# Kernel optimization log

Measured on AMD Instinct MI355X. Metric: run time of the kernel, lower is better.

## Reference

```python
import jax, jax.numpy as jnp
import numpy as np

M = 41
RHO = M / 2.0          # rho=-1 -> M/2
OVERLAPS = 40
STRIDES = 40
N_FFT = OVERLAPS + STRIDES   # 80
HOP = STRIDES                # 40

def _get_index():
    S = []
    for n1 in range(-(M // 2), M // 2):
        for n2 in range(-(M // 2), M // 2):
            if abs(n1 * n2) <= RHO * (M // 2):
                S.append((n1, n2))
    return np.asarray(S, dtype=np.int64)

IDX = _get_index()          # [K,2], K=1600
N1 = IDX[:, 0]
N2 = IDX[:, 1]
K = len(IDX)

def setup_inputs() -> dict:
    key = jax.random.key(0)
    ks = jax.random.split(key, 7)
    b, L, m = 2, 2080, 2
    return {
        "x_real": jax.random.normal(ks[0], (b, L, m), jnp.float32),
        "x_imag": jax.random.normal(ks[1], (b, L, m), jnp.float32),
        "task_info": jax.random.uniform(ks[2], (b, 4), jnp.float32),
        "w_real": jax.random.normal(ks[3], (K,), jnp.float32) * 0.02,
        "w_imag": jax.random.normal(ks[4], (K,), jnp.float32) * 0.02,
        "b_real": jax.random.normal(ks[5], (1,), jnp.float32) * 0.02,
        "b_imag": jax.random.normal(ks[6], (1,), jnp.float32) * 0.02,
    }

def _stft(x):
    # x: [b, L, m] complex -> [b, T, F, m]; rectangular window, center=False
    L = x.shape[1]
    T = (L - N_FFT) // HOP + 1
    idx = np.arange(T)[:, None] * HOP + np.arange(N_FFT)[None, :]
    frames = x[:, idx, :]                      # [b, T, F, m]
    return jnp.fft.fft(frames, axis=2)

def _istft(X, L):
    # X: [b, T, F, m] -> [b, L, m] via overlap-add, rect-window normalization
    frames = jnp.fft.ifft(X, axis=2)
    b, T, F, m = X.shape
    idx = (np.arange(T)[:, None] * HOP + np.arange(F)[None, :]).reshape(-1)
    y = jnp.zeros((b, L, m), X.dtype).at[:, idx, :].add(frames.reshape(b, -1, m))
    cov = np.zeros(L)
    np.add.at(cov, idx, 1.0)
    cov = jnp.asarray(np.where(cov > 0, cov, 1.0), jnp.float32)
    return y / cov[None, :, None]

def reference(x_real, x_imag, task_info, w_real, w_imag, b_real, b_imag):
    x = x_real + 1j * x_imag                   # [b, L, m] complex64
    b, L, m = x.shape
    # get_power: launch power (dBm in task_info[:,0]) -> mW per mode
    P = jnp.power(10.0, task_info[:, 0] / 10.0) / m   # [b]
    X = _stft(x)                               # [b, T, F, m]
    F = N_FFT
    f = np.arange(F)
    g1 = (f[None, :] - N1[:, None]) % F        # [K, F] : torch.roll(X, n1, dims=2)
    g12 = (f[None, :] - (N1 + N2)[:, None]) % F
    g2 = (f[None, :] - N2[:, None]) % F
    # A_k = roll(X,n1) * conj(roll(X,n1+n2))   -> [b, T, K, F, m]
    A = X[:, :, g1, :] * jnp.conj(X[:, :, g12, :])
    A = A + jnp.roll(A, 1, axis=1)             # + previous frame (circular)
    E = A * X[:, :, g2, :]                     # [b, T, K, F, m]
    w = (w_real + 1j * w_imag).astype(E.dtype)
    bias = (b_real[0] + 1j * b_imag[0]).astype(E.dtype)
    delta = jnp.einsum('btkfm,k->btfm', E, w) + bias   # ComplexLinear(K,1)
    d = _istft(delta, L)                       # [b, L, m]
    out = x + d * P[:, None, None].astype(d.dtype)
    return out[:, OVERLAPS // 2: L - OVERLAPS // 2, :]
```

## Files before the change

### kernel.cpp

```cpp
#include <hip/hip_runtime.h>
#include <math.h>

#define BATCH 2
#define LLEN  2080
#define MCH   2
#define TT    51
#define FF    80
#define HOP   40
#define KW    1600
#define OUTL  2040
#define NT    640
#define PI_F  3.14159265358979323846f

__global__ __launch_bounds__(NT) void fused_kernel(
    const float* __restrict__ xr, const float* __restrict__ xi,
    const float* __restrict__ wr, const float* __restrict__ wi,
    const float* __restrict__ br, const float* __restrict__ bi,
    float2* __restrict__ Fr)
{
    __shared__ float2 xs[2 * FF];
    __shared__ float2 tw[FF];
    __shared__ float2 Yt2[2 * FF];
    __shared__ float2 Yp[FF];
    __shared__ float2 Wsh[KW];
    __shared__ float2 Zall[40][2 * FF];
    __shared__ float2 dvec[FF];

    float2* red  = &Zall[0][0];
    float2 (*redD)[FF] = (float2(*)[FF])&Zall[0][0];

    int tid = threadIdx.x;
    int bid = blockIdx.x;
    int b   = bid / (TT * MCH);
    int rem = bid % (TT * MCH);
    int t   = rem / MCH;
    int mi  = rem % MCH;
    int tp  = (t + TT - 1) % TT;

    if (tid < FF) {
        int g = (b * LLEN + t * HOP + tid) * MCH + mi;
        xs[tid] = make_float2(xr[g], xi[g]);
        float s, c;
        sincosf((2.0f * PI_F / FF) * (float)tid, &s, &c);
        tw[tid] = make_float2(c, s);
    } else if (tid < 2 * FF) {
        int j = tid - FF;
        int g = (b * LLEN + tp * HOP + j) * MCH + mi;
        xs[tid] = make_float2(xr[g], xi[g]);
    } else {
        for (int k = tid - 2 * FF; k < KW; k += NT - 2 * FF)
            Wsh[k] = make_float2(wr[k], wi[k]);
    }
    __syncthreads();

    {
        int o    = tid >> 2;
        int part = tid & 3;
        int ff   = o % FF;
        int frm  = o / FF;
        const float2* xb = &xs[frm * FF];
        float2 a = make_float2(0.f, 0.f);
        int j0 = part * 20;
        int r  = (ff * j0) % FF;
        for (int j = j0; j < j0 + 20; ++j) {
            float2 xv = xb[j];
            float2 tv = tw[r];
            a.x += xv.x * tv.x + xv.y * tv.y;
            a.y += xv.y * tv.x - xv.x * tv.y;
            r += ff; if (r >= FF) r -= FF;
        }
        red[part * 160 + o] = a;
    }
    __syncthreads();
    if (tid < 2 * FF) {
        float2 s = make_float2(0.f, 0.f);
        for (int p = 0; p < 4; ++p) {
            float2 v = red[p * 160 + tid];
            s.x += v.x; s.y += v.y;
        }
        if (tid < FF) {
            Yt2[tid + 20] = s;
            Yt2[(tid < 60) ? (tid + 100) : (tid - 60)] = s;
        } else {
            Yp[tid - FF] = s;
        }
    }
    __syncthreads();

    for (int i = 0; i < 5; ++i) {
        int zi = tid + i * NT;
        int jn = zi / FF;
        int g  = zi % FF;
        int n2 = jn - 20;
        int gm = g - n2; if (gm >= FF) gm -= FF; if (gm < 0) gm += FF;
        float2 a  = Yt2[g + 20], bm = Yt2[gm + 20];
        float2 cc = Yp[g],       dm = Yp[gm];
        float zre = a.x * bm.x + a.y * bm.y + cc.x * dm.x + cc.y * dm.y;
        float zim = a.y * bm.x - a.x * bm.y + cc.y * dm.x - cc.x * dm.y;
        float2 z = make_float2(zre, zim);
        Zall[jn][g + 20] = z;
        Zall[jn][(g < 60) ? (g + 100) : (g - 60)] = z;
    }
    __syncthreads();

    float2 o0, o1, o2, o3, o4;
    int jn, fb;
    {
        jn = tid >> 4;
        int fg = tid & 15;
        fb = fg * 5;
        const float2* zz = Zall[jn];

        float2 S0 = make_float2(0.f,0.f), S1 = S0, S2 = S0, S3 = S0, S4 = S0;
        float2 w0 = zz[fb + 40], w1 = zz[fb + 41], w2 = zz[fb + 42],
               w3 = zz[fb + 43], w4 = zz[fb + 44];
        #pragma unroll
        for (int jn1 = 0; jn1 < 40; ++jn1) {
            float2 wv = Wsh[jn1 * 40 + jn];
            S0.x += wv.x * w0.x - wv.y * w0.y;  S0.y += wv.x * w0.y + wv.y * w0.x;
            S1.x += wv.x * w1.x - wv.y * w1.y;  S1.y += wv.x * w1.y + wv.y * w1.x;
            S2.x += wv.x * w2.x - wv.y * w2.y;  S2.y += wv.x * w2.y + wv.y * w2.x;
            S3.x += wv.x * w3.x - wv.y * w3.y;  S3.y += wv.x * w3.y + wv.y * w3.x;
            S4.x += wv.x * w4.x - wv.y * w4.y;  S4.y += wv.x * w4.y + wv.y * w4.x;
            if (jn1 < 39) {
                float2 nv = zz[fb + 39 - jn1];
                w4 = w3; w3 = w2; w2 = w1; w1 = w0; w0 = nv;
            }
        }
        float2 y;
        y = Yt2[fb + 0 - jn + 40]; o0 = make_float2(y.x*S0.x - y.y*S0.y, y.x*S0.y + y.y*S0.x);
        y = Yt2[fb + 1 - jn + 40]; o1 = make_float2(y.x*S1.x - y.y*S1.y, y.x*S1.y + y.y*S1.x);
        y = Yt2[fb + 2 - jn + 40]; o2 = make_float2(y.x*S2.x - y.y*S2.y, y.x*S2.y + y.y*S2.x);
        y = Yt2[fb + 3 - jn + 40]; o3 = make_float2(y.x*S3.x - y.y*S3.y, y.x*S3.y + y.y*S3.x);
        y = Yt2[fb + 4 - jn + 40]; o4 = make_float2(y.x*S4.x - y.y*S4.y, y.x*S4.y + y.y*S4.x);
    }
    __syncthreads();
    redD[jn][fb + 0] = o0;
    redD[jn][fb + 1] = o1;
    redD[jn][fb + 2] = o2;
    redD[jn][fb + 3] = o3;
    redD[jn][fb + 4] = o4;
    __syncthreads();
    if (tid < FF) {
        float2 s = make_float2(br[0], bi[0]);
        for (int p = 0; p < 40; ++p) {
            float2 v = redD[p][tid];
            s.x += v.x; s.y += v.y;
        }
        dvec[tid] = s;
    }
    __syncthreads();

    {
        int j    = tid >> 3;
        int part = tid & 7;
        float2 a = make_float2(0.f, 0.f);
        int f0 = part * 10;
        int r  = (j * f0) % FF;
        for (int ff2 = f0; ff2 < f0 + 10; ++ff2) {
            float2 dv = dvec[ff2];
            float2 tv = tw[r];
            a.x += dv.x * tv.x - dv.y * tv.y;
            a.y += dv.x * tv.y + dv.y * tv.x;
            r += j; if (r >= FF) r -= FF;
        }
        red[part * FF + j] = a;
    }
    __syncthreads();
    if (tid < FF) {
        float2 s = make_float2(0.f, 0.f);
        for (int p = 0; p < 8; ++p) {
            float2 v = red[p * FF + tid];
            s.x += v.x; s.y += v.y;
        }
        s.x *= (1.0f / FF);
        s.y *= (1.0f / FF);
        Fr[((b * TT + t) * MCH + mi) * FF + tid] = s;
    }
}

__global__ void out_kernel(
    const float* __restrict__ xr, const float* __restrict__ xi,
    const float* __restrict__ ti, const float2* __restrict__ Fr,
    float* __restrict__ out, int out_size)
{
    int idx = blockIdx.x * blockDim.x + threadIdx.x;
    int tot = BATCH * OUTL * MCH;
    if (idx >= tot) return;
    int mi  = idx % MCH;
    int rem = idx / MCH;
    int lo  = rem % OUTL;
    int b   = rem / OUTL;
    int l   = lo + 20;

    float P = exp2f(ti[b * 4] * 0.33219280948873623f) * 0.5f;

    int t1 = l / HOP;
    int t0 = t1 - 1;
    float2 acc = make_float2(0.f, 0.f);
    float cov = 0.f;
    if (t1 <= TT - 1) {
        float2 v = Fr[((b * TT + t1) * MCH + mi) * FF + (l - HOP * t1)];
        acc.x += v.x; acc.y += v.y; cov += 1.f;
    }
    if (t0 >= 0) {
        float2 v = Fr[((b * TT + t0) * MCH + mi) * FF + (l - HOP * t0)];
        acc.x += v.x; acc.y += v.y; cov += 1.f;
    }
    float inv = 1.0f / cov;
    acc.x *= inv; acc.y *= inv;

    int gi = (b * LLEN + l) * MCH + mi;
    float outr = xr[gi] + acc.x * P;
    if (out_size == tot) {
        out[idx] = outr;
    } else {
        float outi = xi[gi] + acc.y * P;
        out[idx * 2]     = outr;
        out[idx * 2 + 1] = outi;
    }
}

extern "C" void kernel_launch(void* const* d_in, const int* in_sizes, int n_in,
                              void* d_out, int out_size, void* d_ws, size_t ws_size,
                              hipStream_t stream)
{
    const float* xr = (const float*)d_in[0];
    const float* xi = (const float*)d_in[1];
    const float* ti = (const float*)d_in[2];
    const float* wr = (const float*)d_in[3];
    const float* wi = (const float*)d_in[4];
    const float* br = (const float*)d_in[5];
    const float* bi = (const float*)d_in[6];

    float2* Fr = (float2*)d_ws;

    int nb = BATCH * TT * MCH;
    fused_kernel<<<nb, NT, 0, stream>>>(xr, xi, wr, wi, br, bi, Fr);

    int tot = BATCH * OUTL * MCH;
    out_kernel<<<(tot + 255) / 256, 256, 0, stream>>>(xr, xi, ti, Fr,
                                                      (float*)d_out, out_size);
}
```

Before: 16.96 us.

## Move inverse DFT into output kernel and use recurrence twiddles with shuffle reductions

The inverse DFT of each frame no longer runs in the fused kernel. The output kernel now computes it per output sample: two threads evaluate the two overlapping frames and combine their results with a lane shuffle. The forward DFT builds its twiddles by complex-rotation recurrence instead of reading a shared table, and reduces its partial sums with warp shuffles, which removes one barrier. The K reduction is split into two stages to shorten the serial loop. The aim is to cut barriers and serial work in the big kernel, at the cost of redundant 80-term sums in the second kernel and some recurrence rounding error.

```diff
diff --git a/kernel.cpp b/kernel.cpp
--- a/kernel.cpp
+++ b/kernel.cpp
@@ -10,24 +10,21 @@
 #define KW    1600
 #define OUTL  2040
 #define NT    640
+#define NB    (BATCH * TT * MCH)
 #define PI_F  3.14159265358979323846f
 
-__global__ __launch_bounds__(NT) void fused_kernel(
+__global__ __launch_bounds__(NT) void fused_k1(
     const float* __restrict__ xr, const float* __restrict__ xi,
     const float* __restrict__ wr, const float* __restrict__ wi,
     const float* __restrict__ br, const float* __restrict__ bi,
-    float2* __restrict__ Fr)
+    float2* __restrict__ dvec_g)
 {
     __shared__ float2 xs[2 * FF];
-    __shared__ float2 tw[FF];
     __shared__ float2 Yt2[2 * FF];
     __shared__ float2 Yp[FF];
     __shared__ float2 Wsh[KW];
     __shared__ float2 Zall[40][2 * FF];
-    __shared__ float2 dvec[FF];
-
-    float2* red  = &Zall[0][0];
-    float2 (*redD)[FF] = (float2(*)[FF])&Zall[0][0];
+    float2* flat = &Zall[0][0];
 
     int tid = threadIdx.x;
     int bid = blockIdx.x;
@@ -37,15 +34,10 @@
     int mi  = rem % MCH;
     int tp  = (t + TT - 1) % TT;
 
-    if (tid < FF) {
-        int g = (b * LLEN + t * HOP + tid) * MCH + mi;
-        xs[tid] = make_float2(xr[g], xi[g]);
-        float s, c;
-        sincosf((2.0f * PI_F / FF) * (float)tid, &s, &c);
-        tw[tid] = make_float2(c, s);
-    } else if (tid < 2 * FF) {
-        int j = tid - FF;
-        int g = (b * LLEN + tp * HOP + j) * MCH + mi;
+    if (tid < 2 * FF) {
+        int frm = tid / FF, j = tid % FF;
+        int tt  = frm == 0 ? t : tp;
+        int g = (b * LLEN + tt * HOP + j) * MCH + mi;
         xs[tid] = make_float2(xr[g], xi[g]);
     } else {
         for (int k = tid - 2 * FF; k < KW; k += NT - 2 * FF)
@@ -59,30 +51,36 @@
         int ff   = o % FF;
         int frm  = o / FF;
         const float2* xb = &xs[frm * FF];
+
+        int q = (ff * part) & 3;
+        float2 tv = (q == 0) ? make_float2(1.f, 0.f)
+                  : (q == 1) ? make_float2(0.f, -1.f)
+                  : (q == 2) ? make_float2(-1.f, 0.f)
+                  :            make_float2(0.f, 1.f);
+        float sp, cp;
+        sincosf(-(2.0f * PI_F / FF) * (float)ff, &sp, &cp);
+        float2 st = make_float2(cp, sp);
+
         float2 a = make_float2(0.f, 0.f);
-        int j0 = part * 20;
-        int r  = (ff * j0) % FF;
-        for (int j = j0; j < j0 + 20; ++j) {
+        int j = part * 20;
+        #pragma unroll 4
+        for (int i = 0; i < 20; ++i, ++j) {
             float2 xv = xb[j];
-            float2 tv = tw[r];
-            a.x += xv.x * tv.x + xv.y * tv.y;
-            a.y += xv.y * tv.x - xv.x * tv.y;
-            r += ff; if (r >= FF) r -= FF;
-        }
-        red[part * 160 + o] = a;
-    }
-    __syncthreads();
-    if (tid < 2 * FF) {
-        float2 s = make_float2(0.f, 0.f);
-        for (int p = 0; p < 4; ++p) {
-            float2 v = red[p * 160 + tid];
-            s.x += v.x; s.y += v.y;
-        }
-        if (tid < FF) {
-            Yt2[tid + 20] = s;
-            Yt2[(tid < 60) ? (tid + 100) : (tid - 60)] = s;
-        } else {
-            Yp[tid - FF] = s;
+            a.x += xv.x * tv.x - xv.y * tv.y;
+            a.y += xv.x * tv.y + xv.y * tv.x;
+            float nx = tv.x * st.x - tv.y * st.y;
+            tv.y = tv.x * st.y + tv.y * st.x;
+            tv.x = nx;
+        }
+        a.x += __shfl_xor(a.x, 1); a.y += __shfl_xor(a.y, 1);
+        a.x += __shfl_xor(a.x, 2); a.y += __shfl_xor(a.y, 2);
+        if (part == 0) {
+            if (o < FF) {
+                Yt2[o + 20] = a;
+                Yt2[(o < 60) ? (o + 100) : (o - 60)] = a;
+            } else {
+                Yp[o - FF] = a;
+            }
         }
     }
     __syncthreads();
@@ -135,89 +133,90 @@
         y = Yt2[fb + 4 - jn + 40]; o4 = make_float2(y.x*S4.x - y.y*S4.y, y.x*S4.y + y.y*S4.x);
     }
     __syncthreads();
-    redD[jn][fb + 0] = o0;
-    redD[jn][fb + 1] = o1;
-    redD[jn][fb + 2] = o2;
-    redD[jn][fb + 3] = o3;
-    redD[jn][fb + 4] = o4;
+    flat[jn * FF + fb + 0] = o0;
+    flat[jn * FF + fb + 1] = o1;
+    flat[jn * FF + fb + 2] = o2;
+    flat[jn * FF + fb + 3] = o3;
+    flat[jn * FF + fb + 4] = o4;
+    __syncthreads();
+
+    {
+        int f = tid % FF;
+        int p = tid / FF;
+        float2 s = make_float2(0.f, 0.f);
+        for (int q2 = 0; q2 < 5; ++q2) {
+            float2 v = flat[(p * 5 + q2) * FF + f];
+            s.x += v.x; s.y += v.y;
+        }
+        flat[3200 + p * FF + f] = s;
+    }
     __syncthreads();
     if (tid < FF) {
         float2 s = make_float2(br[0], bi[0]);
-        for (int p = 0; p < 40; ++p) {
-            float2 v = redD[p][tid];
+        for (int p = 0; p < 8; ++p) {
+            float2 v = flat[3200 + p * FF + tid];
             s.x += v.x; s.y += v.y;
         }
-        dvec[tid] = s;
-    }
-    __syncthreads();
-
-    {
-        int j    = tid >> 3;
-        int part = tid & 7;
-        float2 a = make_float2(0.f, 0.f);
-        int f0 = part * 10;
-        int r  = (j * f0) % FF;
-        for (int ff2 = f0; ff2 < f0 + 10; ++ff2) {
-            float2 dv = dvec[ff2];
-            float2 tv = tw[r];
-            a.x += dv.x * tv.x - dv.y * tv.y;
-            a.y += dv.x * tv.y + dv.y * tv.x;
-            r += j; if (r >= FF) r -= FF;
-        }
-        red[part * FF + j] = a;
-    }
-    __syncthreads();
-    if (tid < FF) {
-        float2 s = make_float2(0.f, 0.f);
-        for (int p = 0; p < 8; ++p) {
-            float2 v = red[p * FF + tid];
-            s.x += v.x; s.y += v.y;
-        }
-        s.x *= (1.0f / FF);
-        s.y *= (1.0f / FF);
-        Fr[((b * TT + t) * MCH + mi) * FF + tid] = s;
+        dvec_g[((b * TT + t) * MCH + mi) * FF + tid] = s;
     }
 }
 
-__global__ void out_kernel(
+__global__ void out_k2(
     const float* __restrict__ xr, const float* __restrict__ xi,
-    const float* __restrict__ ti, const float2* __restrict__ Fr,
+    const float* __restrict__ ti, const float2* __restrict__ dvec_g,
     float* __restrict__ out, int out_size)
 {
-    int idx = blockIdx.x * blockDim.x + threadIdx.x;
-    int tot = BATCH * OUTL * MCH;
-    if (idx >= tot) return;
-    int mi  = idx % MCH;
-    int rem = idx / MCH;
-    int lo  = rem % OUTL;
-    int b   = rem / OUTL;
-    int l   = lo + 20;
-
-    float P = exp2f(ti[b * 4] * 0.33219280948873623f) * 0.5f;
-
-    int t1 = l / HOP;
-    int t0 = t1 - 1;
-    float2 acc = make_float2(0.f, 0.f);
-    float cov = 0.f;
-    if (t1 <= TT - 1) {
-        float2 v = Fr[((b * TT + t1) * MCH + mi) * FF + (l - HOP * t1)];
-        acc.x += v.x; acc.y += v.y; cov += 1.f;
-    }
-    if (t0 >= 0) {
-        float2 v = Fr[((b * TT + t0) * MCH + mi) * FF + (l - HOP * t0)];
-        acc.x += v.x; acc.y += v.y; cov += 1.f;
-    }
-    float inv = 1.0f / cov;
-    acc.x *= inv; acc.y *= inv;
-
-    int gi = (b * LLEN + l) * MCH + mi;
-    float outr = xr[gi] + acc.x * P;
-    if (out_size == tot) {
-        out[idx] = outr;
-    } else {
-        float outi = xi[gi] + acc.y * P;
-        out[idx * 2]     = outr;
-        out[idx * 2 + 1] = outi;
+    const int tot = BATCH * OUTL * MCH;
+    int idx2 = blockIdx.x * blockDim.x + threadIdx.x;
+    bool active = idx2 < 2 * tot;
+
+    float cx = 0.f, cy = 0.f, cov = 0.f;
+    int p = 0, h = 0, b = 0, mi = 0, l = 0;
+    if (active) {
+        p  = idx2 >> 1;
+        h  = idx2 & 1;
+        mi = p % MCH;
+        int rem = p / MCH;
+        int lo  = rem % OUTL;
+        b  = rem / OUTL;
+        l  = lo + 20;
+        int t1 = l / HOP;
+        int tf = (h == 0) ? t1 : t1 - 1;
+        if (tf >= 0 && tf <= TT - 1) {
+            int j = l - HOP * tf;
+            const float2* dv = &dvec_g[((b * TT + tf) * MCH + mi) * FF];
+            float ss, cc;
+            sincosf((2.0f * PI_F / FF) * (float)j, &ss, &cc);
+            float2 st = make_float2(cc, ss);
+            float2 tv = make_float2(1.f, 0.f);
+            #pragma unroll 4
+            for (int f = 0; f < FF; ++f) {
+                float2 d = dv[f];
+                cx += d.x * tv.x - d.y * tv.y;
+                cy += d.x * tv.y + d.y * tv.x;
+                float nx = tv.x * st.x - tv.y * st.y;
+                tv.y = tv.x * st.y + tv.y * st.x;
+                tv.x = nx;
+            }
+            cov = 1.f;
+        }
+    }
+    cx  += __shfl_xor(cx, 1);
+    cy  += __shfl_xor(cy, 1);
+    cov += __shfl_xor(cov, 1);
+
+    if (active && h == 0) {
+        float P   = exp2f(ti[b * 4] * 0.33219280948873623f) * 0.5f;
+        float inv = 1.0f / ((float)FF * cov);
+        float ar = cx * inv, ai = cy * inv;
+        int gi = (b * LLEN + l) * MCH + mi;
+        float outr = xr[gi] + ar * P;
+        if (out_size == tot) {
+            out[p] = outr;
+        } else {
+            out[p * 2]     = outr;
+            out[p * 2 + 1] = xi[gi] + ai * P;
+        }
     }
 }
 
@@ -233,12 +232,11 @@
     const float* br = (const float*)d_in[5];
     const float* bi = (const float*)d_in[6];
 
-    float2* Fr = (float2*)d_ws;
-
-    int nb = BATCH * TT * MCH;
-    fused_kernel<<<nb, NT, 0, stream>>>(xr, xi, wr, wi, br, bi, Fr);
-
-    int tot = BATCH * OUTL * MCH;
-    out_kernel<<<(tot + 255) / 256, 256, 0, stream>>>(xr, xi, ti, Fr,
-                                                      (float*)d_out, out_size);
+    float2* dvec_g = (float2*)d_ws;
+
+    fused_k1<<<NB, NT, 0, stream>>>(xr, xi, wr, wi, br, bi, dvec_g);
+
+    int nthr = 2 * BATCH * OUTL * MCH;
+    out_k2<<<(nthr + 255) / 256, 256, 0, stream>>>(xr, xi, ti, dvec_g,
+                                                   (float*)d_out, out_size);
 }
```

After: 21.40 us. 1.26x slower.
